# Kernel optimization log

Hardware: AMD Instinct MI355X
Metric: run time of the kernel (lower is better)

Reference implementation:

```python
import jax, jax.numpy as jnp
import numpy as np
from jax import lax

D_MODEL = 256
D_STATE = 16
BATCH = 4
SEQ = 16384
LN_EPS = 1e-5


def setup_inputs() -> dict:
    key = jax.random.key(0)
    ks = jax.random.split(key, 16)
    d, s = D_MODEL, D_STATE
    lim = 1.0 / np.sqrt(d)
    u = lambda k, shape, l: jax.random.uniform(k, shape, jnp.float32, -l, l)
    return {
        "x": jax.random.normal(ks[0], (BATCH, SEQ, d), jnp.float32),
        # forward branch params (torch Linear stored as (in, out))
        "W_fproj": u(ks[1], (d, 2 * d), lim),
        "b_fproj": u(ks[2], (2 * d,), lim),
        "A_f": jax.random.normal(ks[3], (s, d), jnp.float32),
        "W_fgate": u(ks[4], (d, s), lim),
        "b_fgate": u(ks[5], (s,), lim),
        # backward branch params
        "W_bproj": u(ks[6], (d, 2 * d), lim),
        "b_bproj": u(ks[7], (2 * d,), lim),
        "A_b": jax.random.normal(ks[8], (s, d), jnp.float32),
        "W_bgate": u(ks[9], (d, s), lim),
        "b_bgate": u(ks[10], (s,), lim),
        # output proj + layernorm
        "W_out": u(ks[11], (2 * d, d), 1.0 / np.sqrt(2 * d)),
        "b_out": u(ks[12], (d,), 1.0 / np.sqrt(2 * d)),
        "ln_g": jnp.ones((d,), jnp.float32),
        "ln_b": jnp.zeros((d,), jnp.float32),
    }


def _scan_dir(x, W_proj, b_proj, A, W_gate, b_gate):
    """One direction: gated state-space scan. x: (B,S,D) -> (B,S,D)."""
    B, S, D = x.shape
    proj = x @ W_proj + b_proj            # (B,S,2D)
    value = proj[..., D:]                 # the 'gate' chunk is unused in the original
    gw = jax.nn.sigmoid(value @ W_gate + b_gate)  # (B,S,d_state)

    def step(state, inp):
        g, v = inp                        # g:(B,Ns), v:(B,D)
        gi = g[:, :, None]                # (B,Ns,1)
        upd = A[None, :, :] * v[:, None, :]
        state = state * gi + upd * (1.0 - gi)
        out = (state * gi).sum(axis=1)    # (B,D)
        return state, out

    init = jnp.zeros((B, A.shape[0], D), x.dtype)
    _, outs = lax.scan(step, init, (gw.transpose(1, 0, 2), value.transpose(1, 0, 2)))
    return outs.transpose(1, 0, 2)        # (B,S,D)


def reference(x, W_fproj, b_fproj, A_f, W_fgate, b_fgate,
              W_bproj, b_bproj, A_b, W_bgate, b_bgate,
              W_out, b_out, ln_g, ln_b):
    fwd = _scan_dir(x, W_fproj, b_fproj, A_f, W_fgate, b_fgate)
    x_rev = jnp.flip(x, axis=1)
    bwd = jnp.flip(_scan_dir(x_rev, W_bproj, b_bproj, A_b, W_bgate, b_bgate), axis=1)
    combined = jnp.concatenate([fwd, bwd], axis=-1)    # (B,S,2D)
    out = combined @ W_out + b_out                     # (B,S,D)
    mu = out.mean(axis=-1, keepdims=True)
    var = out.var(axis=-1, keepdims=True)
    out = (out - mu) * lax.rsqrt(var + LN_EPS) * ln_g + ln_b
    return out  # dropout is identity in eval mode
```

## Files before the change

kernel.cpp:

```cpp
#include <hip/hip_runtime.h>

#define SEQ   16384
#define NB    4
#define NROWS 65536
#define NC    512
#define CL    32

typedef short bf16x8 __attribute__((ext_vector_type(8)));
typedef float f32x4  __attribute__((ext_vector_type(4)));
typedef float f32x2  __attribute__((ext_vector_type(2)));

__device__ inline float bf2f(ushort u) {
    unsigned int t = ((unsigned int)u) << 16;
    float f; __builtin_memcpy(&f, &t, 4); return f;
}
__device__ inline ushort f2bf(float f) {
    unsigned int b; __builtin_memcpy(&b, &f, 4);
    unsigned int r = (b + 0x7FFFu + ((b >> 16) & 1u)) >> 16;
    return (ushort)r;
}

__global__ __launch_bounds__(256) void prep_weights(
    const float* __restrict__ Wf, const float* __restrict__ Wb,
    const float* __restrict__ Wo, const float* __restrict__ Wgf,
    const float* __restrict__ Wgb, const float* __restrict__ bfp,
    const float* __restrict__ bbp,
    ushort* __restrict__ BTv, ushort* __restrict__ WoT,
    ushort* __restrict__ WgT, float* __restrict__ bias_v)
{
    int idx = blockIdx.x * 256 + threadIdx.x;
    if (idx < 131072) {
        int dir = idx >> 16, j = idx & 65535, n = j >> 8, k = j & 255;
        const float* W = dir ? Wb : Wf;
        BTv[idx] = f2bf(W[k * 512 + 256 + n]);
    } else if (idx < 262144) {
        int j = idx - 131072; int n = j >> 9, k = j & 511;
        WoT[j] = f2bf(Wo[k * 256 + n]);
    } else if (idx < 270336) {
        int j = idx - 262144; int dir = j >> 12, jj = j & 4095, s = jj >> 8, k = jj & 255;
        WgT[j] = f2bf((dir ? Wgb : Wgf)[k * 16 + s]);
    } else if (idx < 270848) {
        int j = idx - 270336; int dir = j >> 8, n = j & 255;
        bias_v[j] = (dir ? bbp : bfp)[256 + n];
    }
}

__global__ __launch_bounds__(512) void gemm_value(
    const float* __restrict__ x, const ushort* __restrict__ BTv,
    const float* __restrict__ bias_v, ushort* __restrict__ value)
{
    __shared__ ushort Al[128 * 40];
    __shared__ ushort Bl[256 * 40];
    const int tid = threadIdx.x;
    const int m0 = blockIdx.x * 128, dir = blockIdx.y;
    const ushort* BT = BTv + dir * 65536;
    const int w = tid >> 6, l = tid & 63;
    const int wr = w >> 2, wc = w & 3;
    const int l15 = l & 15, lk = (l >> 4) * 8;
    f32x4 acc[4][4] = {};

    for (int kk = 0; kk < 256; kk += 32) {
        {
            int r = tid >> 2, c = (tid & 3) * 8;
            const float* xp = x + (size_t)(m0 + r) * 256 + kk + c;
            float4 a = *(const float4*)xp;
            float4 b = *(const float4*)(xp + 4);
            ushort u[8];
            u[0] = f2bf(a.x); u[1] = f2bf(a.y); u[2] = f2bf(a.z); u[3] = f2bf(a.w);
            u[4] = f2bf(b.x); u[5] = f2bf(b.y); u[6] = f2bf(b.z); u[7] = f2bf(b.w);
            *(uint4*)&Al[r * 40 + c] = *(uint4*)u;
        }
        #pragma unroll
        for (int i = 0; i < 2; ++i) {
            int idx = tid + i * 512; int r = idx >> 2, c = idx & 3;
            *(uint4*)&Bl[r * 40 + c * 8] = *(const uint4*)(BT + (size_t)r * 256 + kk + c * 8);
        }
        __syncthreads();
        bf16x8 af[4], bfr[4];
        #pragma unroll
        for (int m = 0; m < 4; ++m) af[m] = *(const bf16x8*)&Al[(wr * 64 + m * 16 + l15) * 40 + lk];
        #pragma unroll
        for (int n = 0; n < 4; ++n) bfr[n] = *(const bf16x8*)&Bl[(wc * 64 + n * 16 + l15) * 40 + lk];
        #pragma unroll
        for (int m = 0; m < 4; ++m)
            #pragma unroll
            for (int n = 0; n < 4; ++n)
                acc[m][n] = __builtin_amdgcn_mfma_f32_16x16x32_bf16(af[m], bfr[n], acc[m][n], 0, 0, 0);
        __syncthreads();
    }
    const int rbase = (l >> 4) * 4;
    #pragma unroll
    for (int m = 0; m < 4; ++m)
        #pragma unroll
        for (int n = 0; n < 4; ++n) {
            int col = wc * 64 + n * 16 + l15;
            float bv = bias_v[dir * 256 + col];
            #pragma unroll
            for (int r = 0; r < 4; ++r) {
                int row = m0 + wr * 64 + m * 16 + rbase + r;
                value[(size_t)row * 512 + dir * 256 + col] = f2bf(acc[m][n][r] + bv);
            }
        }
}

__global__ __launch_bounds__(256, 3) void gate_scan(
    const ushort* __restrict__ value, const ushort* __restrict__ WgT,
    const float* __restrict__ bgf, const float* __restrict__ bgb,
    float* __restrict__ gw, float* __restrict__ L, float* __restrict__ P)
{
    __shared__ ushort Av[64 * 264];
    __shared__ float gsm[64 * 16];
    const int tid = threadIdx.x;
    const int r0 = blockIdx.x * 64, dir = blockIdx.y;
    #pragma unroll
    for (int i = 0; i < 8; ++i) {
        int idx = tid + i * 256; int r = idx >> 5, c = idx & 31;
        *(uint4*)&Av[r * 264 + c * 8] =
            *(const uint4*)(value + (size_t)(r0 + r) * 512 + dir * 256 + c * 8);
    }
    __syncthreads();
    const int w = tid >> 6, l = tid & 63, l15 = l & 15, lk = (l >> 4) * 8;
    const ushort* Wg = WgT + dir * 4096;
    f32x4 acc = {};
    #pragma unroll
    for (int kk = 0; kk < 256; kk += 32) {
        bf16x8 af = *(const bf16x8*)&Av[(w * 16 + l15) * 264 + kk + lk];
        bf16x8 bf = *(const bf16x8*)(Wg + l15 * 256 + kk + lk);
        acc = __builtin_amdgcn_mfma_f32_16x16x32_bf16(af, bf, acc, 0, 0, 0);
    }
    const float bgs = (dir ? bgb : bgf)[l15];
    const int rbase = (l >> 4) * 4;
    const int b = r0 >> 14, t0 = r0 & 16383;
    #pragma unroll
    for (int r = 0; r < 4; ++r) {
        int lr = w * 16 + rbase + r;
        float sv = 1.f / (1.f + __expf(-(acc[r] + bgs)));
        gsm[lr * 16 + l15] = sv;
        gw[((size_t)(dir * NB + b) * SEQ + t0 + lr) * 16 + l15] = sv;
    }
    __syncthreads();
    const int ci = tid >> 7, dp = tid & 127;
    const int chunk = (t0 >> 5) + ci;
    f32x2 c[16] = {};
    for (int i = 0; i < CL; ++i) {
        int row = dir ? (CL - 1 - i) : i;
        uint vv = *(const uint*)&Av[(ci * 32 + row) * 264 + dp * 2];
        f32x2 v; v.x = bf2f((ushort)(vv & 0xffffu)); v.y = bf2f((ushort)(vv >> 16));
        float g[16];
        #pragma unroll
        for (int q = 0; q < 4; ++q)
            *(float4*)&g[q * 4] = *(const float4*)&gsm[(ci * 32 + row) * 16 + q * 4];
        #pragma unroll
        for (int s = 0; s < 16; ++s) {
            f32x2 gg; gg.x = g[s]; gg.y = g[s];
            c[s] = v + gg * (c[s] - v);
        }
    }
    float* Lp = L + ((size_t)(dir * NB + b) * NC + chunk) * 4096 + dp * 2;
    #pragma unroll
    for (int s = 0; s < 16; ++s)
        *(f32x2*)(Lp + s * 256) = c[s];
    if (dp < 16) {
        float p = 1.f;
        for (int t = 0; t < CL; ++t) p *= gsm[(ci * 32 + t) * 16 + dp];
        P[((size_t)(dir * NB + b) * NC + chunk) * 16 + dp] = p;
    }
}

__global__ __launch_bounds__(128, 2) void chunk_scan(
    float* __restrict__ L, const float* __restrict__ P)
{
    const int bid = blockIdx.x;
    const int dir = bid >> 7, b = (bid >> 5) & 3, s = (bid >> 1) & 15, dh = bid & 1;
    const int d = dh * 128 + threadIdx.x;
    const size_t cb = (size_t)(dir * NB + b) * NC;
    float* Lb = L + cb * 4096 + s * 256 + d;
    const float* Pb = P + cb * 16 + s;
    float e = 0.f;
    float lA[16], pA[16], lB[16], pB[16];

#define LOADB(la, pa, ib) { _Pragma("unroll") \
    for (int j = 0; j < 16; ++j) { \
        int t = (ib) * 16 + j; int k = dir ? (NC - 1 - t) : t; \
        la[j] = Lb[(size_t)k * 4096]; pa[j] = Pb[k * 16]; } }
#define PROCB(la, pa, ib) { _Pragma("unroll") \
    for (int j = 0; j < 16; ++j) { \
        int t = (ib) * 16 + j; int k = dir ? (NC - 1 - t) : t; \
        Lb[(size_t)k * 4096] = e; e = pa[j] * e + la[j]; } }

    LOADB(lA, pA, 0)
    for (int ib = 0; ib < 32; ib += 2) {
        LOADB(lB, pB, ib + 1)
        PROCB(lA, pA, ib)
        if (ib + 2 < 32) { LOADB(lA, pA, ib + 2) }
        PROCB(lB, pB, ib + 1)
    }
#undef LOADB
#undef PROCB
}

__global__ __launch_bounds__(128, 3) void pass_c(
    ushort* __restrict__ value, const float* __restrict__ gw,
    const float* __restrict__ L, const float* __restrict__ A_f,
    const float* __restrict__ A_b)
{
    const int chunk = blockIdx.x, b = blockIdx.y, dir = blockIdx.z;
    const int tid = threadIdx.x;
    __shared__ float gs[CL * 16];
    const float* gwd = gw + ((size_t)(dir * NB + b) * SEQ + chunk * CL) * 16;
    ((float4*)gs)[tid] = ((const float4*)gwd)[tid];
    __syncthreads();
    ushort* vb = value + ((size_t)b * SEQ + chunk * CL) * 512 + dir * 256 + tid * 2;
    const float* Ad = dir ? A_b : A_f;
    const float* Lp = L + ((size_t)(dir * NB + b) * NC + chunk) * 4096 + tid * 2;
    f32x2 a[16], c[16];
    #pragma unroll
    for (int s = 0; s < 16; ++s) {
        a[s] = *(const f32x2*)(Ad + s * 256 + tid * 2);
        c[s] = *(const f32x2*)(Lp + s * 256);
    }
    uint vbuf[4];
    #pragma unroll
    for (int j = 0; j < 4; ++j) {
        int row = dir ? (CL - 1 - j) : j;
        vbuf[j] = *(const uint*)(vb + (size_t)row * 512);
    }
    for (int i0 = 0; i0 < CL; i0 += 4) {
        uint vcur[4];
        #pragma unroll
        for (int j = 0; j < 4; ++j) vcur[j] = vbuf[j];
        if (i0 + 4 < CL) {
            #pragma unroll
            for (int j = 0; j < 4; ++j) {
                int t = i0 + 4 + j;
                int row = dir ? (CL - 1 - t) : t;
                vbuf[j] = *(const uint*)(vb + (size_t)row * 512);
            }
        }
        #pragma unroll
        for (int j = 0; j < 4; ++j) {
            int t = i0 + j;
            int row = dir ? (CL - 1 - t) : t;
            f32x2 v; v.x = bf2f((ushort)(vcur[j] & 0xffffu)); v.y = bf2f((ushort)(vcur[j] >> 16));
            float g[16];
            #pragma unroll
            for (int q = 0; q < 4; ++q)
                *(float4*)&g[q * 4] = *(const float4*)&gs[row * 16 + q * 4];
            f32x2 o = {0.f, 0.f};
            #pragma unroll
            for (int s = 0; s < 16; ++s) {
                f32x2 gg; gg.x = g[s]; gg.y = g[s];
                c[s] = v + gg * (c[s] - v);
                o += a[s] * (gg * c[s]);
            }
            uint outv = (uint)f2bf(o.x) | ((uint)f2bf(o.y) << 16);
            *(uint*)(vb + (size_t)row * 512) = outv;
        }
    }
}

__global__ __launch_bounds__(512) void gemm_out_ln(
    const ushort* __restrict__ A, const ushort* __restrict__ BT,
    const float* __restrict__ b_out, const float* __restrict__ ln_g,
    const float* __restrict__ ln_b, float* __restrict__ out)
{
    __shared__ ushort Al[128 * 40];
    __shared__ ushort Bl[256 * 40];
    __shared__ float red[2][2][4][64];
    const int tid = threadIdx.x;
    const int m0 = blockIdx.x * 128;
    const int w = tid >> 6, l = tid & 63;
    const int wr = w >> 2, wc = w & 3;
    const int l15 = l & 15, lk = (l >> 4) * 8;
    f32x4 acc[4][4] = {};

    for (int kk = 0; kk < 512; kk += 32) {
        {
            int r = tid >> 2, c = tid & 3;
            *(uint4*)&Al[r * 40 + c * 8] = *(const uint4*)(A + (size_t)(m0 + r) * 512 + kk + c * 8);
        }
        #pragma unroll
        for (int i = 0; i < 2; ++i) {
            int idx = tid + i * 512; int r = idx >> 2, c = idx & 3;
            *(uint4*)&Bl[r * 40 + c * 8] = *(const uint4*)(BT + (size_t)r * 512 + kk + c * 8);
        }
        __syncthreads();
        bf16x8 af[4], bfr[4];
        #pragma unroll
        for (int m = 0; m < 4; ++m) af[m] = *(const bf16x8*)&Al[(wr * 64 + m * 16 + l15) * 40 + lk];
        #pragma unroll
        for (int n = 0; n < 4; ++n) bfr[n] = *(const bf16x8*)&Bl[(wc * 64 + n * 16 + l15) * 40 + lk];
        #pragma unroll
        for (int m = 0; m < 4; ++m)
            #pragma unroll
            for (int n = 0; n < 4; ++n)
                acc[m][n] = __builtin_amdgcn_mfma_f32_16x16x32_bf16(af[m], bfr[n], acc[m][n], 0, 0, 0);
        __syncthreads();
    }
    const int rbase = (l >> 4) * 4;
    float gg[4], bb[4];
    #pragma unroll
    for (int n = 0; n < 4; ++n) {
        int col = wc * 64 + n * 16 + l15;
        float bv = b_out[col];
        gg[n] = ln_g[col]; bb[n] = ln_b[col];
        #pragma unroll
        for (int m = 0; m < 4; ++m)
            #pragma unroll
            for (int r = 0; r < 4; ++r)
                acc[m][n][r] += bv;
    }
    float s1[4][4], s2[4][4];
    #pragma unroll
    for (int m = 0; m < 4; ++m)
        #pragma unroll
        for (int r = 0; r < 4; ++r) {
            float a_ = 0.f, b_ = 0.f;
            #pragma unroll
            for (int n = 0; n < 4; ++n) {
                float v = acc[m][n][r];
                a_ += v; b_ += v * v;
            }
            s1[m][r] = a_; s2[m][r] = b_;
        }
    #pragma unroll
    for (int mask = 1; mask < 16; mask <<= 1)
        #pragma unroll
        for (int m = 0; m < 4; ++m)
            #pragma unroll
            for (int r = 0; r < 4; ++r) {
                s1[m][r] += __shfl_xor(s1[m][r], mask, 64);
                s2[m][r] += __shfl_xor(s2[m][r], mask, 64);
            }
    if (l15 == 0) {
        #pragma unroll
        for (int m = 0; m < 4; ++m)
            #pragma unroll
            for (int r = 0; r < 4; ++r) {
                int row = m * 16 + rbase + r;
                red[0][wr][wc][row] = s1[m][r];
                red[1][wr][wc][row] = s2[m][r];
            }
    }
    __syncthreads();
    #pragma unroll
    for (int m = 0; m < 4; ++m)
        #pragma unroll
        for (int r = 0; r < 4; ++r) {
            int row = m * 16 + rbase + r;
            float t1 = red[0][wr][0][row] + red[0][wr][1][row] + red[0][wr][2][row] + red[0][wr][3][row];
            float t2 = red[1][wr][0][row] + red[1][wr][1][row] + red[1][wr][2][row] + red[1][wr][3][row];
            float mu = t1 * (1.f / 256.f);
            float var = t2 * (1.f / 256.f) - mu * mu;
            float rs = rsqrtf(var + 1e-5f);
            #pragma unroll
            for (int n = 0; n < 4; ++n) {
                int col = wc * 64 + n * 16 + l15;
                out[(size_t)(m0 + wr * 64 + row) * 256 + col] = (acc[m][n][r] - mu) * rs * gg[n] + bb[n];
            }
        }
}

extern "C" void kernel_launch(void* const* d_in, const int* in_sizes, int n_in,
                              void* d_out, int out_size, void* d_ws, size_t ws_size,
                              hipStream_t stream)
{
    const float* x       = (const float*)d_in[0];
    const float* W_fproj = (const float*)d_in[1];
    const float* b_fproj = (const float*)d_in[2];
    const float* A_f     = (const float*)d_in[3];
    const float* W_fgate = (const float*)d_in[4];
    const float* b_fgate = (const float*)d_in[5];
    const float* W_bproj = (const float*)d_in[6];
    const float* b_bproj = (const float*)d_in[7];
    const float* A_b     = (const float*)d_in[8];
    const float* W_bgate = (const float*)d_in[9];
    const float* b_bgate = (const float*)d_in[10];
    const float* W_out   = (const float*)d_in[11];
    const float* b_out   = (const float*)d_in[12];
    const float* ln_g    = (const float*)d_in[13];
    const float* ln_b    = (const float*)d_in[14];

    char* ws = (char*)d_ws;
    ushort* value  = (ushort*)(ws + 0);
    float*  gw     = (float*) (ws + 67108864);
    float*  L      = (float*) (ws + 75497472);
    float*  P      = (float*) (ws + 142606336);
    ushort* BTv    = (ushort*)(ws + 142868480);
    ushort* WoT    = (ushort*)(ws + 143130624);
    ushort* WgT    = (ushort*)(ws + 143392768);
    float*  bias_v = (float*) (ws + 143409152);

    prep_weights<<<1058, 256, 0, stream>>>(W_fproj, W_bproj, W_out, W_fgate, W_bgate,
                                           b_fproj, b_bproj, BTv, WoT, WgT, bias_v);
    gemm_value<<<dim3(512, 2), 512, 0, stream>>>(x, BTv, bias_v, value);
    gate_scan<<<dim3(1024, 2), 256, 0, stream>>>(value, WgT, b_fgate, b_bgate, gw, L, P);
    chunk_scan<<<256, 128, 0, stream>>>(L, P);
    pass_c<<<dim3(NC, NB, 2), 128, 0, stream>>>(value, gw, L, A_f, A_b);
    gemm_out_ln<<<512, 512, 0, stream>>>(value, WoT, b_out, ln_g, ln_b, (float*)d_out);
}
```

Before: 207.3 us.

## Store chunk-scan carry states in bf16 with d-major layout and pre-transposed A

The per-chunk local states L are now written as bf16 instead of fp32, which halves the traffic through gate_scan, chunk_scan and pass_c. The layout changes so each d-pair's 16 states are contiguous, and chunk_scan is remapped so one block covers all 16 states for a group of 256 entries. pass_c reads a pre-transposed A prepared once in prep_weights and gets a higher occupancy bound. Rounding carries to bf16 adds precision loss in the recurrence.

```diff
diff --git a/kernel.cpp b/kernel.cpp
--- a/kernel.cpp
+++ b/kernel.cpp
@@ -14,6 +14,12 @@
     unsigned int t = ((unsigned int)u) << 16;
     float f; __builtin_memcpy(&f, &t, 4); return f;
 }
+__device__ inline float bflo(uint u) {
+    uint t = u << 16; float f; __builtin_memcpy(&f, &t, 4); return f;
+}
+__device__ inline float bfhi(uint u) {
+    uint t = u & 0xffff0000u; float f; __builtin_memcpy(&f, &t, 4); return f;
+}
 __device__ inline ushort f2bf(float f) {
     unsigned int b; __builtin_memcpy(&b, &f, 4);
     unsigned int r = (b + 0x7FFFu + ((b >> 16) & 1u)) >> 16;
@@ -24,9 +30,11 @@
     const float* __restrict__ Wf, const float* __restrict__ Wb,
     const float* __restrict__ Wo, const float* __restrict__ Wgf,
     const float* __restrict__ Wgb, const float* __restrict__ bfp,
-    const float* __restrict__ bbp,
+    const float* __restrict__ bbp, const float* __restrict__ A_f,
+    const float* __restrict__ A_b,
     ushort* __restrict__ BTv, ushort* __restrict__ WoT,
-    ushort* __restrict__ WgT, float* __restrict__ bias_v)
+    ushort* __restrict__ WgT, float* __restrict__ bias_v,
+    float* __restrict__ AsT)
 {
     int idx = blockIdx.x * 256 + threadIdx.x;
     if (idx < 131072) {
@@ -42,6 +50,9 @@
     } else if (idx < 270848) {
         int j = idx - 270336; int dir = j >> 8, n = j & 255;
         bias_v[j] = (dir ? bbp : bfp)[256 + n];
+    } else if (idx < 279040) {
+        int j = idx - 270848; int dir = j >> 12, jj = j & 4095, d = jj >> 4, s = jj & 15;
+        AsT[j] = (dir ? A_b : A_f)[s * 256 + d];
     }
 }
 
@@ -106,7 +117,7 @@
 __global__ __launch_bounds__(256, 3) void gate_scan(
     const ushort* __restrict__ value, const ushort* __restrict__ WgT,
     const float* __restrict__ bgf, const float* __restrict__ bgb,
-    float* __restrict__ gw, float* __restrict__ L, float* __restrict__ P)
+    float* __restrict__ gw, ushort* __restrict__ L16, float* __restrict__ P)
 {
     __shared__ ushort Av[64 * 264];
     __shared__ float gsm[64 * 16];
@@ -145,7 +156,7 @@
     for (int i = 0; i < CL; ++i) {
         int row = dir ? (CL - 1 - i) : i;
         uint vv = *(const uint*)&Av[(ci * 32 + row) * 264 + dp * 2];
-        f32x2 v; v.x = bf2f((ushort)(vv & 0xffffu)); v.y = bf2f((ushort)(vv >> 16));
+        f32x2 v; v.x = bflo(vv); v.y = bfhi(vv);
         float g[16];
         #pragma unroll
         for (int q = 0; q < 4; ++q)
@@ -156,10 +167,15 @@
             c[s] = v + gg * (c[s] - v);
         }
     }
-    float* Lp = L + ((size_t)(dir * NB + b) * NC + chunk) * 4096 + dp * 2;
-    #pragma unroll
-    for (int s = 0; s < 16; ++s)
-        *(f32x2*)(Lp + s * 256) = c[s];
+    {
+        ushort ub[32];
+        #pragma unroll
+        for (int s = 0; s < 16; ++s) { ub[s] = f2bf(c[s].x); ub[16 + s] = f2bf(c[s].y); }
+        ushort* Lp = L16 + ((size_t)(dir * NB + b) * NC + chunk) * 4096 + dp * 32;
+        #pragma unroll
+        for (int q = 0; q < 4; ++q)
+            *(uint4*)(Lp + q * 8) = *(uint4*)&ub[q * 8];
+    }
     if (dp < 16) {
         float p = 1.f;
         for (int t = 0; t < CL; ++t) p *= gsm[(ci * 32 + t) * 16 + dp];
@@ -167,17 +183,19 @@
     }
 }
 
-__global__ __launch_bounds__(128, 2) void chunk_scan(
-    float* __restrict__ L, const float* __restrict__ P)
+__global__ __launch_bounds__(256, 2) void chunk_scan(
+    ushort* __restrict__ L16, const float* __restrict__ P)
 {
     const int bid = blockIdx.x;
-    const int dir = bid >> 7, b = (bid >> 5) & 3, s = (bid >> 1) & 15, dh = bid & 1;
-    const int d = dh * 128 + threadIdx.x;
+    const int dir = bid >> 6, b = (bid >> 4) & 3, dgrp = bid & 15;
+    const int tid = threadIdx.x;
+    const int s = tid & 15;
     const size_t cb = (size_t)(dir * NB + b) * NC;
-    float* Lb = L + cb * 4096 + s * 256 + d;
+    ushort* Lb = L16 + cb * 4096 + dgrp * 256 + tid;
     const float* Pb = P + cb * 16 + s;
     float e = 0.f;
-    float lA[16], pA[16], lB[16], pB[16];
+    ushort lA[16], lB[16];
+    float pA[16], pB[16];
 
 #define LOADB(la, pa, ib) { _Pragma("unroll") \
     for (int j = 0; j < 16; ++j) { \
@@ -186,7 +204,7 @@
 #define PROCB(la, pa, ib) { _Pragma("unroll") \
     for (int j = 0; j < 16; ++j) { \
         int t = (ib) * 16 + j; int k = dir ? (NC - 1 - t) : t; \
-        Lb[(size_t)k * 4096] = e; e = pa[j] * e + la[j]; } }
+        Lb[(size_t)k * 4096] = f2bf(e); e = pa[j] * e + bf2f(la[j]); } }
 
     LOADB(lA, pA, 0)
     for (int ib = 0; ib < 32; ib += 2) {
@@ -199,10 +217,9 @@
 #undef PROCB
 }
 
-__global__ __launch_bounds__(128, 3) void pass_c(
+__global__ __launch_bounds__(128, 4) void pass_c(
     ushort* __restrict__ value, const float* __restrict__ gw,
-    const float* __restrict__ L, const float* __restrict__ A_f,
-    const float* __restrict__ A_b)
+    const ushort* __restrict__ L16, const float* __restrict__ AsT)
 {
     const int chunk = blockIdx.x, b = blockIdx.y, dir = blockIdx.z;
     const int tid = threadIdx.x;
@@ -211,13 +228,17 @@
     ((float4*)gs)[tid] = ((const float4*)gwd)[tid];
     __syncthreads();
     ushort* vb = value + ((size_t)b * SEQ + chunk * CL) * 512 + dir * 256 + tid * 2;
-    const float* Ad = dir ? A_b : A_f;
-    const float* Lp = L + ((size_t)(dir * NB + b) * NC + chunk) * 4096 + tid * 2;
-    f32x2 a[16], c[16];
-    #pragma unroll
-    for (int s = 0; s < 16; ++s) {
-        a[s] = *(const f32x2*)(Ad + s * 256 + tid * 2);
-        c[s] = *(const f32x2*)(Lp + s * 256);
+    const float* Ad = AsT + dir * 4096 + tid * 32;
+    const ushort* Lp = L16 + ((size_t)(dir * NB + b) * NC + chunk) * 4096 + tid * 32;
+    f32x2 a0[8], a1[8], c0[8], c1[8];
+    #pragma unroll
+    for (int sp = 0; sp < 8; ++sp) {
+        a0[sp] = *(const f32x2*)(Ad + sp * 2);
+        a1[sp] = *(const f32x2*)(Ad + 16 + sp * 2);
+        uint u0 = *(const uint*)(Lp + sp * 2);
+        uint u1 = *(const uint*)(Lp + 16 + sp * 2);
+        c0[sp].x = bflo(u0); c0[sp].y = bfhi(u0);
+        c1[sp].x = bflo(u1); c1[sp].y = bfhi(u1);
     }
     uint vbuf[4];
     #pragma unroll
@@ -241,19 +262,19 @@
         for (int j = 0; j < 4; ++j) {
             int t = i0 + j;
             int row = dir ? (CL - 1 - t) : t;
-            f32x2 v; v.x = bf2f((ushort)(vcur[j] & 0xffffu)); v.y = bf2f((ushort)(vcur[j] >> 16));
-            float g[16];
-            #pragma unroll
-            for (int q = 0; q < 4; ++q)
-                *(float4*)&g[q * 4] = *(const float4*)&gs[row * 16 + q * 4];
-            f32x2 o = {0.f, 0.f};
-            #pragma unroll
-            for (int s = 0; s < 16; ++s) {
-                f32x2 gg; gg.x = g[s]; gg.y = g[s];
-                c[s] = v + gg * (c[s] - v);
-                o += a[s] * (gg * c[s]);
-            }
-            uint outv = (uint)f2bf(o.x) | ((uint)f2bf(o.y) << 16);
+            float v0 = bflo(vcur[j]), v1 = bfhi(vcur[j]);
+            f32x2 vd0; vd0.x = v0; vd0.y = v0;
+            f32x2 vd1; vd1.x = v1; vd1.y = v1;
+            f32x2 o0 = {0.f, 0.f}, o1 = {0.f, 0.f};
+            #pragma unroll
+            for (int sp = 0; sp < 8; ++sp) {
+                f32x2 g = *(const f32x2*)&gs[row * 16 + sp * 2];
+                c0[sp] = vd0 + g * (c0[sp] - vd0);
+                o0 += (a0[sp] * g) * c0[sp];
+                c1[sp] = vd1 + g * (c1[sp] - vd1);
+                o1 += (a1[sp] * g) * c1[sp];
+            }
+            uint outv = (uint)f2bf(o0.x + o0.y) | ((uint)f2bf(o1.x + o1.y) << 16);
             *(uint*)(vb + (size_t)row * 512) = outv;
         }
     }
@@ -384,18 +405,20 @@
     char* ws = (char*)d_ws;
     ushort* value  = (ushort*)(ws + 0);
     float*  gw     = (float*) (ws + 67108864);
-    float*  L      = (float*) (ws + 75497472);
-    float*  P      = (float*) (ws + 142606336);
-    ushort* BTv    = (ushort*)(ws + 142868480);
-    ushort* WoT    = (ushort*)(ws + 143130624);
-    ushort* WgT    = (ushort*)(ws + 143392768);
-    float*  bias_v = (float*) (ws + 143409152);
-
-    prep_weights<<<1058, 256, 0, stream>>>(W_fproj, W_bproj, W_out, W_fgate, W_bgate,
-                                           b_fproj, b_bproj, BTv, WoT, WgT, bias_v);
+    ushort* L16    = (ushort*)(ws + 75497472);
+    float*  P      = (float*) (ws + 109051904);
+    ushort* BTv    = (ushort*)(ws + 109314048);
+    ushort* WoT    = (ushort*)(ws + 109576192);
+    ushort* WgT    = (ushort*)(ws + 109838336);
+    float*  bias_v = (float*) (ws + 109854720);
+    float*  AsT    = (float*) (ws + 109856768);
+
+    prep_weights<<<1090, 256, 0, stream>>>(W_fproj, W_bproj, W_out, W_fgate, W_bgate,
+                                           b_fproj, b_bproj, A_f, A_b,
+                                           BTv, WoT, WgT, bias_v, AsT);
     gemm_value<<<dim3(512, 2), 512, 0, stream>>>(x, BTv, bias_v, value);
-    gate_scan<<<dim3(1024, 2), 256, 0, stream>>>(value, WgT, b_fgate, b_bgate, gw, L, P);
-    chunk_scan<<<256, 128, 0, stream>>>(L, P);
-    pass_c<<<dim3(NC, NB, 2), 128, 0, stream>>>(value, gw, L, A_f, A_b);
+    gate_scan<<<dim3(1024, 2), 256, 0, stream>>>(value, WgT, b_fgate, b_bgate, gw, L16, P);
+    chunk_scan<<<128, 256, 0, stream>>>(L16, P);
+    pass_c<<<dim3(NC, NB, 2), 128, 0, stream>>>(value, gw, L16, AsT);
     gemm_out_ln<<<512, 512, 0, stream>>>(value, WoT, b_out, ln_g, ln_b, (float*)d_out);
 }
```

New measurement: 201.8 us. 1.03x faster.
